# Kernel tuning notes

Measured on AMD Instinct MI355X. Metric: run time of the kernel, lower is better.

The kernel has to match this reference:

```python
import jax, jax.numpy as jnp
import numpy as np


def setup_inputs() -> dict:
    key = jax.random.key(0)
    ks = jax.random.split(key, 8)
    B, C, D, H, W = 4, 256, 16, 16, 16
    C8 = C // 8
    x = jax.random.normal(ks[0], (B, C, D, H, W), dtype=jnp.float32)
    # 1x1x1 conv weights == per-channel linear maps
    Wq = jax.random.normal(ks[1], (C8, C), dtype=jnp.float32) * (1.0 / np.sqrt(C))
    bq = jax.random.normal(ks[2], (C8,), dtype=jnp.float32) * 0.01
    Wk = jax.random.normal(ks[3], (C8, C), dtype=jnp.float32) * (1.0 / np.sqrt(C))
    bk = jax.random.normal(ks[4], (C8,), dtype=jnp.float32) * 0.01
    Wv = jax.random.normal(ks[5], (C, C), dtype=jnp.float32) * (1.0 / np.sqrt(C))
    bv = jax.random.normal(ks[6], (C,), dtype=jnp.float32) * 0.01
    gamma = jax.random.normal(ks[7], (1,), dtype=jnp.float32) * 0.1
    return {"x": x, "Wq": Wq, "bq": bq, "Wk": Wk, "bk": bk,
            "Wv": Wv, "bv": bv, "gamma": gamma}


def reference(x, Wq, bq, Wk, bk, Wv, bv, gamma):
    B, C, D, H, W = x.shape
    N = D * H * W
    xf = x.reshape(B, C, N)  # (B, C, N)
    # 1x1x1 convs == channel-wise linear projections
    q = jnp.einsum('qc,bcn->bnq', Wq, xf) + bq            # (B, N, C/8)
    k = jnp.einsum('kc,bcn->bkn', Wk, xf) + bk[:, None]   # (B, C/8, N)
    v = jnp.einsum('vc,bcn->bvn', Wv, xf) + bv[:, None]   # (B, C, N)
    energy = jnp.einsum('bnc,bcm->bnm', q, k)             # (B, N, N), NO 1/sqrt(d) scaling (as in source)
    attention = jax.nn.softmax(energy, axis=-1)           # softmax over keys
    # out[b,c,m] = sum_n V[b,c,n] * A[b,m,n]  (torch: bmm(V, A^T))
    out = jnp.einsum('bcn,bmn->bcm', v, attention)        # (B, C, N)
    out = out.reshape(B, C, D, H, W)
    return gamma[0] * out + x
```

## Files before the change

kernel.cpp:

```cpp
#include <hip/hip_runtime.h>
#include <hip/hip_bf16.h>
#include <math.h>

#define BATCH 4
#define CH    256
#define NPOS  4096
#define DQK   32
#define SHIFT 20.0f

typedef __attribute__((ext_vector_type(8))) short bf16x8;
typedef __attribute__((ext_vector_type(4))) float f32x4;

static __device__ __forceinline__ unsigned int pack_bf2(float a, float b) {
    __hip_bfloat162 h = __float22bfloat162_rn(make_float2(a, b));
    return *reinterpret_cast<unsigned int*>(&h);
}
static __device__ __forceinline__ unsigned short f2bf1(float f) {
    unsigned int u = __float_as_uint(f);
    u += 0x7fff + ((u >> 16) & 1);
    return (unsigned short)(u >> 16);
}
static __device__ __forceinline__ bf16x8 pack8(const float* v) {
    bf16x8 r;
    #pragma unroll
    for (int j = 0; j < 8; ++j) r[j] = (short)f2bf1(v[j]);
    return r;
}

static __device__ __forceinline__ void lds_barrier() {
    asm volatile("s_waitcnt lgkmcnt(0)" ::: "memory");
    __builtin_amdgcn_s_barrier();
    asm volatile("" ::: "memory");
}

__global__ __launch_bounds__(256) void qkv_proj_mfma(
    const float* __restrict__ x,
    const float* __restrict__ Wq, const float* __restrict__ bq,
    const float* __restrict__ Wk, const float* __restrict__ bk,
    const float* __restrict__ Wv, const float* __restrict__ bv,
    __hip_bfloat16* __restrict__ qb, __hip_bfloat16* __restrict__ kb,
    __hip_bfloat16* __restrict__ vb)
{
    const int tid  = threadIdx.x;
    const int wave = tid >> 6, lane = tid & 63;
    const int g    = lane >> 4, lm = lane & 15;
    const int n0   = blockIdx.x * 32;
    const int b    = blockIdx.y;
    const float* xb = x + (size_t)b * CH * NPOS;

    bf16x8 xf[2][8];
    #pragma unroll
    for (int nt = 0; nt < 2; ++nt)
        #pragma unroll
        for (int kt = 0; kt < 8; ++kt) {
            const float* p = xb + (32 * kt + 8 * g) * NPOS + n0 + 16 * nt + lm;
            float v[8];
            #pragma unroll
            for (int j = 0; j < 8; ++j) v[j] = p[j * NPOS];
            xf[nt][kt] = pack8(v);
        }

    #pragma unroll
    for (int s = 0; s < 5; ++s) {
        const int cot = wave * 5 + s;
        const float* Wsrc; const float* bsrc; int cbase; int kind;
        if (cot < 2)      { Wsrc = Wq; bsrc = bq; cbase = cot * 16;      kind = 0; }
        else if (cot < 4) { Wsrc = Wk; bsrc = bk; cbase = cot * 16 - 32; kind = 1; }
        else              { Wsrc = Wv; bsrc = bv; cbase = cot * 16 - 64; kind = 2; }

        bf16x8 wf[8];
        const float* wrow = Wsrc + (size_t)(cbase + lm) * CH;
        #pragma unroll
        for (int kt = 0; kt < 8; ++kt) {
            float4 wa = *(const float4*)(wrow + 32 * kt + 8 * g);
            float4 wc = *(const float4*)(wrow + 32 * kt + 8 * g + 4);
            float wv[8] = {wa.x, wa.y, wa.z, wa.w, wc.x, wc.y, wc.z, wc.w};
            wf[kt] = pack8(wv);
        }
        const float4 b4 = *(const float4*)(bsrc + cbase + 4 * g);
        f32x4 a0 = {b4.x, b4.y, b4.z, b4.w};
        f32x4 a1 = a0;
        #pragma unroll
        for (int kt = 0; kt < 8; ++kt) {
            a0 = __builtin_amdgcn_mfma_f32_16x16x32_bf16(wf[kt], xf[0][kt], a0, 0, 0, 0);
            a1 = __builtin_amdgcn_mfma_f32_16x16x32_bf16(wf[kt], xf[1][kt], a1, 0, 0, 0);
        }

        if (kind <= 1) {
            __hip_bfloat16* dst = (kind == 0 ? qb : kb);
            #pragma unroll
            for (int nt = 0; nt < 2; ++nt) {
                f32x4 a = nt ? a1 : a0;
                int n = n0 + 16 * nt + lm;
                uint2 w;
                w.x = pack_bf2(a[0], a[1]);
                w.y = pack_bf2(a[2], a[3]);
                *(uint2*)(dst + ((size_t)b * NPOS + n) * DQK + cbase + 4 * g) = w;
            }
        } else {
            #pragma unroll
            for (int nt = 0; nt < 2; ++nt) {
                f32x4 a = nt ? a1 : a0;
                int n = n0 + 16 * nt + lm;
                int n64 = n >> 6, half = (n >> 5) & 1, nin = n & 31;
                #pragma unroll
                for (int r = 0; r < 4; ++r) {
                    int c = cbase + 4 * g + r;
                    size_t off = (((size_t)b * 16 + (c >> 4)) * 64 + n64) * 1024
                               + (size_t)half * 512 + (c & 15) * 32 + nin;
                    *reinterpret_cast<unsigned short*>(vb + off) = f2bf1(a[r]);
                }
            }
        }
    }
}

__global__ __launch_bounds__(512) void flash_pam_kernel(
    const __hip_bfloat16* __restrict__ qb, const __hip_bfloat16* __restrict__ kb,
    const __hip_bfloat16* __restrict__ vb, const float* __restrict__ x,
    const float* __restrict__ gamma, float* __restrict__ out)
{
    __shared__ alignas(16) unsigned char Pl[2][8192];
    __shared__ float lred[4][4][16];

    const int tid  = threadIdx.x;
    const int wave = tid >> 6;
    const int lane = tid & 63;
    const int g    = lane >> 4;
    const int lm   = lane & 15;
    const int bid  = blockIdx.x;
    const int b    = bid & 3;
    const int m0   = (bid >> 2) * 64;
    const int kt   = wave & 3;
    const int mtA  = (wave >> 2) * 2;
    const unsigned swz = (unsigned)(lm & 7) << 4;

    const bf16x8 qfA = *reinterpret_cast<const bf16x8*>(
        qb + ((size_t)b * NPOS + m0 + 16 * mtA + lm) * DQK + 8 * g);
    const bf16x8 qfB = *reinterpret_cast<const bf16x8*>(
        qb + ((size_t)b * NPOS + m0 + 16 * mtA + 16 + lm) * DQK + 8 * g);

    const __hip_bfloat16* kbb = kb + (size_t)b * NPOS * DQK;
    const int koff0 = (16 * kt + lm) * DQK + 8 * g;
    const __hip_bfloat16* vbb = vb + (size_t)b * 16 * 64 * 1024;
    int vfb[4];
    #pragma unroll
    for (int cti = 0; cti < 2; ++cti)
        #pragma unroll
        for (int kc = 0; kc < 2; ++kc)
            vfb[2 * cti + kc] = (2 * wave + cti) * 65536 + kc * 512 + lm * 32 + 8 * g;

    const unsigned wbA = (unsigned)(16 * mtA + lm) * 128
                       + (((unsigned)(32 * kt + 8 * g)) ^ swz);
    const unsigned wbB = wbA + 16 * 128;

    unsigned char* P0 = &Pl[0][0];
    unsigned char* P1 = &Pl[1][0];

    f32x4 acc[2][4];
    #pragma unroll
    for (int i = 0; i < 2; ++i)
        #pragma unroll
        for (int j = 0; j < 4; ++j) acc[i][j] = (f32x4){0.f, 0.f, 0.f, 0.f};
    float lsA = 0.f, lsB = 0.f;

#define LOADK(dst, tk_) \
    dst = *reinterpret_cast<const bf16x8*>(kbb + koff0 + (tk_) * 2048);

#define LOADV(dst, tv_) { \
    _Pragma("unroll") for (int f = 0; f < 4; ++f) \
        dst[f] = *reinterpret_cast<const bf16x8*>(vbb + vfb[f] + (tv_) * 1024); }

#define QKW(KU, PW) { \
    f32x4 z = {0.f, 0.f, 0.f, 0.f}; \
    f32x4 sA = __builtin_amdgcn_mfma_f32_16x16x32_bf16(KU, qfA, z, 0, 0, 0); \
    f32x4 sB = __builtin_amdgcn_mfma_f32_16x16x32_bf16(KU, qfB, z, 0, 0, 0); \
    { float p0 = __expf(sA[0] - SHIFT), p1 = __expf(sA[1] - SHIFT); \
      float p2 = __expf(sA[2] - SHIFT), p3 = __expf(sA[3] - SHIFT); \
      lsA += (p0 + p1) + (p2 + p3); \
      uint2 w; w.x = pack_bf2(p0, p1); w.y = pack_bf2(p2, p3); \
      *reinterpret_cast<uint2*>((PW) + wbA) = w; } \
    { float p0 = __expf(sB[0] - SHIFT), p1 = __expf(sB[1] - SHIFT); \
      float p2 = __expf(sB[2] - SHIFT), p3 = __expf(sB[3] - SHIFT); \
      lsB += (p0 + p1) + (p2 + p3); \
      uint2 w; w.x = pack_bf2(p0, p1); w.y = pack_bf2(p2, p3); \
      *reinterpret_cast<uint2*>((PW) + wbB) = w; } }

#define PV(PR, VR) { \
    _Pragma("unroll") for (int kc = 0; kc < 2; ++kc) { \
        bf16x8 pf[4]; \
        _Pragma("unroll") for (int mt = 0; mt < 4; ++mt) \
            pf[mt] = *reinterpret_cast<const bf16x8*>( \
                (PR) + (unsigned)(16 * mt + lm) * 128 \
                     + (((unsigned)(kc * 64 + 16 * g)) ^ swz)); \
        __builtin_amdgcn_s_setprio(1); \
        _Pragma("unroll") for (int cti = 0; cti < 2; ++cti) \
            _Pragma("unroll") for (int mt = 0; mt < 4; ++mt) \
                acc[cti][mt] = __builtin_amdgcn_mfma_f32_16x16x32_bf16( \
                    VR[2 * cti + kc], pf[mt], acc[cti][mt], 0, 0, 0); \
        __builtin_amdgcn_s_setprio(0); } }

#define BODY(t_, PR, PW, VR, VL, KU, KL) { \
    { int tv = (t_) + 1; if (tv > 63) tv = 63; LOADV(VL, tv); } \
    { int tk2 = (t_) + 2; if (tk2 > 63) tk2 = 63; LOADK(KL, tk2); } \
    QKW(KU, PW); \
    PV(PR, VR); \
    lds_barrier(); }

    bf16x8 kA, kB, vA[4], vB[4];
    LOADK(kA, 0);
    LOADV(vA, 0);
    LOADK(kB, 1);
    QKW(kA, P0);
    lds_barrier();

    for (int it = 0; it < 31; ++it) {
        BODY(2 * it,     P0, P1, vA, vB, kB, kA);
        BODY(2 * it + 1, P1, P0, vB, vA, kA, kB);
    }
    BODY(62, P0, P1, vA, vB, kB, kA);
    PV(P1, vB);

    lsA += __shfl_xor(lsA, 16); lsA += __shfl_xor(lsA, 32);
    lsB += __shfl_xor(lsB, 16); lsB += __shfl_xor(lsB, 32);
    if (lane < 16) {
        lred[kt][mtA][lm]     = lsA;
        lred[kt][mtA + 1][lm] = lsB;
    }
    __syncthreads();

    float linv[4];
    #pragma unroll
    for (int mt = 0; mt < 4; ++mt)
        linv[mt] = 1.f / (lred[0][mt][lm] + lred[1][mt][lm]
                        + lred[2][mt][lm] + lred[3][mt][lm]);

    const float gmv = gamma[0];
    #pragma unroll
    for (int cti = 0; cti < 2; ++cti)
        #pragma unroll
        for (int mt = 0; mt < 4; ++mt)
            #pragma unroll
            for (int r = 0; r < 4; ++r) {
                int c = 32 * wave + 16 * cti + 4 * g + r;
                size_t idx = ((size_t)b * CH + c) * NPOS + m0 + 16 * mt + lm;
                out[idx] = gmv * (acc[cti][mt][r] * linv[mt]) + x[idx];
            }
#undef BODY
#undef PV
#undef QKW
#undef LOADV
#undef LOADK
}

extern "C" void kernel_launch(void* const* d_in, const int* in_sizes, int n_in,
                              void* d_out, int out_size, void* d_ws, size_t ws_size,
                              hipStream_t stream) {
    const float* x  = (const float*)d_in[0];
    const float* Wq = (const float*)d_in[1];
    const float* bq = (const float*)d_in[2];
    const float* Wk = (const float*)d_in[3];
    const float* bk = (const float*)d_in[4];
    const float* Wv = (const float*)d_in[5];
    const float* bv = (const float*)d_in[6];
    const float* gm = (const float*)d_in[7];
    float* out = (float*)d_out;

    __hip_bfloat16* qbuf = (__hip_bfloat16*)d_ws;
    __hip_bfloat16* kbuf = qbuf + (size_t)BATCH * NPOS * DQK;
    __hip_bfloat16* vbuf = kbuf + (size_t)BATCH * NPOS * DQK;

    qkv_proj_mfma<<<dim3(NPOS / 32, BATCH), 256, 0, stream>>>(
        x, Wq, bq, Wk, bk, Wv, bv, qbuf, kbuf, vbuf);
    flash_pam_kernel<<<dim3(NPOS / 64 * BATCH), 512, 0, stream>>>(
        qbuf, kbuf, vbuf, x, gm, out);
}
```

Baseline: 75.10 us.

## Process two key tiles per barrier with doubled P buffers

The flash-attention main loop now handles two 64-key tiles per iteration. It writes both P tiles into a doubled LDS buffer and runs both PV passes before a single barrier, which halves the number of barriers per key. K is prefetched further ahead, and V tiles for the next pair are loaded in advance. This uses more LDS and more registers for the extra V/K prefetch buffers, which may lower occupancy or cause spills.

After: 77.14 us. 2.7% more time.

```diff
diff --git a/kernel.cpp b/kernel.cpp
--- a/kernel.cpp
+++ b/kernel.cpp
@@ -120,7 +120,7 @@
     const __hip_bfloat16* __restrict__ vb, const float* __restrict__ x,
     const float* __restrict__ gamma, float* __restrict__ out)
 {
-    __shared__ alignas(16) unsigned char Pl[2][8192];
+    __shared__ alignas(16) unsigned char Pl[2][2][8192];
     __shared__ float lred[4][4][16];
 
     const int tid  = threadIdx.x;
@@ -154,8 +154,8 @@
                        + (((unsigned)(32 * kt + 8 * g)) ^ swz);
     const unsigned wbB = wbA + 16 * 128;
 
-    unsigned char* P0 = &Pl[0][0];
-    unsigned char* P1 = &Pl[1][0];
+    unsigned char* P0 = &Pl[0][0][0];
+    unsigned char* P1 = &Pl[1][0][0];
 
     f32x4 acc[2][4];
     #pragma unroll
@@ -167,7 +167,7 @@
 #define LOADK(dst, tk_) \
     dst = *reinterpret_cast<const bf16x8*>(kbb + koff0 + (tk_) * 2048);
 
-#define LOADV(dst, tv_) { \
+#define LOADV4(dst, tv_) { \
     _Pragma("unroll") for (int f = 0; f < 4; ++f) \
         dst[f] = *reinterpret_cast<const bf16x8*>(vbb + vfb[f] + (tv_) * 1024); }
 
@@ -186,13 +186,13 @@
       uint2 w; w.x = pack_bf2(p0, p1); w.y = pack_bf2(p2, p3); \
       *reinterpret_cast<uint2*>((PW) + wbB) = w; } }
 
-#define PV(PR, VR) { \
+#define PVt(PRb, VR) { \
+    bf16x8 pf[4]; \
     _Pragma("unroll") for (int kc = 0; kc < 2; ++kc) { \
-        bf16x8 pf[4]; \
         _Pragma("unroll") for (int mt = 0; mt < 4; ++mt) \
             pf[mt] = *reinterpret_cast<const bf16x8*>( \
-                (PR) + (unsigned)(16 * mt + lm) * 128 \
-                     + (((unsigned)(kc * 64 + 16 * g)) ^ swz)); \
+                (PRb) + (unsigned)(16 * mt + lm) * 128 \
+                      + (((unsigned)(kc * 64 + 16 * g)) ^ swz)); \
         __builtin_amdgcn_s_setprio(1); \
         _Pragma("unroll") for (int cti = 0; cti < 2; ++cti) \
             _Pragma("unroll") for (int mt = 0; mt < 4; ++mt) \
@@ -200,26 +200,33 @@
                     VR[2 * cti + kc], pf[mt], acc[cti][mt], 0, 0, 0); \
         __builtin_amdgcn_s_setprio(0); } }
 
-#define BODY(t_, PR, PW, VR, VL, KU, KL) { \
-    { int tv = (t_) + 1; if (tv > 63) tv = 63; LOADV(VL, tv); } \
-    { int tk2 = (t_) + 2; if (tk2 > 63) tk2 = 63; LOADK(KL, tk2); } \
-    QKW(KU, PW); \
-    PV(PR, VR); \
+#define BODY2(t_, PR, PW, VRa, VRb, VLa, VLb, KU0, KU1, KL0, KL1) { \
+    LOADV4(VLa, (t_) + 2); \
+    LOADV4(VLb, (t_) + 3); \
+    { int tk = (t_) + 4; if (tk > 63) tk = 63; LOADK(KL0, tk); } \
+    { int tk = (t_) + 5; if (tk > 63) tk = 63; LOADK(KL1, tk); } \
+    QKW(KU0, PW); \
+    QKW(KU1, (PW) + 8192); \
+    PVt(PR, VRa); \
+    PVt((PR) + 8192, VRb); \
     lds_barrier(); }
 
-    bf16x8 kA, kB, vA[4], vB[4];
-    LOADK(kA, 0);
-    LOADV(vA, 0);
-    LOADK(kB, 1);
-    QKW(kA, P0);
+    bf16x8 k0, k1, k2, k3, vA0[4], vA1[4], vB0[4], vB1[4];
+    LOADK(k0, 0); LOADK(k1, 1);
+    LOADV4(vA0, 0); LOADV4(vA1, 1);
+    LOADK(k2, 2); LOADK(k3, 3);
+    QKW(k0, P0);
+    QKW(k1, P0 + 8192);
     lds_barrier();
 
-    for (int it = 0; it < 31; ++it) {
-        BODY(2 * it,     P0, P1, vA, vB, kB, kA);
-        BODY(2 * it + 1, P1, P0, vB, vA, kA, kB);
+    for (int it = 0; it < 15; ++it) {
+        const int t4 = 4 * it;
+        BODY2(t4,     P0, P1, vA0, vA1, vB0, vB1, k2, k3, k0, k1);
+        BODY2(t4 + 2, P1, P0, vB0, vB1, vA0, vA1, k0, k1, k2, k3);
     }
-    BODY(62, P0, P1, vA, vB, kB, kA);
-    PV(P1, vB);
+    BODY2(60, P0, P1, vA0, vA1, vB0, vB1, k2, k3, k0, k1);
+    PVt(P1, vB0);
+    PVt(P1 + 8192, vB1);
 
     lsA += __shfl_xor(lsA, 16); lsA += __shfl_xor(lsA, 32);
     lsB += __shfl_xor(lsB, 16); lsB += __shfl_xor(lsB, 32);
@@ -246,10 +253,10 @@
                 size_t idx = ((size_t)b * CH + c) * NPOS + m0 + 16 * mt + lm;
                 out[idx] = gmv * (acc[cti][mt][r] * linv[mt]) + x[idx];
             }
-#undef BODY
-#undef PV
+#undef BODY2
+#undef PVt
 #undef QKW
-#undef LOADV
+#undef LOADV4
 #undef LOADK
 }
 
```

## Stage K/V tiles via global_load_lds DMA and fold softmax shift into exp2

Applied to the files above, without the earlier changes.

Replaces the register-prefetched K and V loads in the flash kernel with direct global-to-LDS DMA (global_load_lds) into per-wave staging buffers, which are then read back from LDS each iteration. The aim is to cut VGPR pressure from the double-buffered register prefetch and let the DMA overlap compute. Separately, Q is pre-scaled by log2(e) in the projection kernel and the softmax shift is folded into the MFMA accumulator init, so exp becomes a bare exp2 with no subtraction. The costs are extra LDS use (about 40KB), a vmcnt(0) wait at the top of each iteration that exposes load latency, and a single-buffered staging area.

Measured after the change: 82.24 us. 1.1x slower.

```diff
diff --git a/kernel.cpp b/kernel.cpp
--- a/kernel.cpp
+++ b/kernel.cpp
@@ -6,7 +6,8 @@
 #define CH    256
 #define NPOS  4096
 #define DQK   32
-#define SHIFT 20.0f
+#define LOG2E 1.4426950408889634f
+#define QB2   (-28.853900817779268f)
 
 typedef __attribute__((ext_vector_type(8))) short bf16x8;
 typedef __attribute__((ext_vector_type(4))) float f32x4;
@@ -31,6 +32,16 @@
     asm volatile("s_waitcnt lgkmcnt(0)" ::: "memory");
     __builtin_amdgcn_s_barrier();
     asm volatile("" ::: "memory");
+}
+#define VWAIT0() do { asm volatile("s_waitcnt vmcnt(0)" ::: "memory"); \
+                      __builtin_amdgcn_sched_barrier(0); } while (0)
+#define LGKM0()  do { asm volatile("s_waitcnt lgkmcnt(0)" ::: "memory"); \
+                      __builtin_amdgcn_sched_barrier(0); } while (0)
+
+static __device__ __forceinline__ void dma16(const __hip_bfloat16* g, unsigned char* l) {
+    __builtin_amdgcn_global_load_lds(
+        (const __attribute__((address_space(1))) void*)g,
+        (__attribute__((address_space(3))) void*)l, 16, 0, 0);
 }
 
 __global__ __launch_bounds__(256) void qkv_proj_mfma(
@@ -85,6 +96,10 @@
             a0 = __builtin_amdgcn_mfma_f32_16x16x32_bf16(wf[kt], xf[0][kt], a0, 0, 0, 0);
             a1 = __builtin_amdgcn_mfma_f32_16x16x32_bf16(wf[kt], xf[1][kt], a1, 0, 0, 0);
         }
+        if (kind == 0) {
+            #pragma unroll
+            for (int r = 0; r < 4; ++r) { a0[r] *= LOG2E; a1[r] *= LOG2E; }
+        }
 
         if (kind <= 1) {
             __hip_bfloat16* dst = (kind == 0 ? qb : kb);
@@ -121,6 +136,8 @@
     const float* __restrict__ gamma, float* __restrict__ out)
 {
     __shared__ alignas(16) unsigned char Pl[2][8192];
+    __shared__ alignas(16) unsigned char Vst[8][4096];
+    __shared__ alignas(16) unsigned char Kst[8][1024];
     __shared__ float lred[4][4][16];
 
     const int tid  = threadIdx.x;
@@ -134,26 +151,27 @@
     const int kt   = wave & 3;
     const int mtA  = (wave >> 2) * 2;
     const unsigned swz = (unsigned)(lm & 7) << 4;
+    const unsigned lane16 = (unsigned)lane * 16;
 
     const bf16x8 qfA = *reinterpret_cast<const bf16x8*>(
         qb + ((size_t)b * NPOS + m0 + 16 * mtA + lm) * DQK + 8 * g);
     const bf16x8 qfB = *reinterpret_cast<const bf16x8*>(
         qb + ((size_t)b * NPOS + m0 + 16 * mtA + 16 + lm) * DQK + 8 * g);
 
-    const __hip_bfloat16* kbb = kb + (size_t)b * NPOS * DQK;
-    const int koff0 = (16 * kt + lm) * DQK + 8 * g;
+    const __hip_bfloat16* kgl = kb + (size_t)b * NPOS * DQK + (16 * kt + lm) * DQK + 8 * g;
     const __hip_bfloat16* vbb = vb + (size_t)b * 16 * 64 * 1024;
-    int vfb[4];
+    const __hip_bfloat16* vgl[4];
     #pragma unroll
     for (int cti = 0; cti < 2; ++cti)
         #pragma unroll
         for (int kc = 0; kc < 2; ++kc)
-            vfb[2 * cti + kc] = (2 * wave + cti) * 65536 + kc * 512 + lm * 32 + 8 * g;
+            vgl[2 * cti + kc] = vbb + (2 * wave + cti) * 65536 + kc * 512 + lm * 32 + 8 * g;
+    unsigned char* vdst = &Vst[wave][0];
+    unsigned char* kdst = &Kst[wave][0];
 
     const unsigned wbA = (unsigned)(16 * mtA + lm) * 128
                        + (((unsigned)(32 * kt + 8 * g)) ^ swz);
     const unsigned wbB = wbA + 16 * 128;
-
     unsigned char* P0 = &Pl[0][0];
     unsigned char* P1 = &Pl[1][0];
 
@@ -164,29 +182,31 @@
         for (int j = 0; j < 4; ++j) acc[i][j] = (f32x4){0.f, 0.f, 0.f, 0.f};
     float lsA = 0.f, lsB = 0.f;
 
-#define LOADK(dst, tk_) \
-    dst = *reinterpret_cast<const bf16x8*>(kbb + koff0 + (tk_) * 2048);
-
-#define LOADV(dst, tv_) { \
+#define DMAK(t_) dma16(kgl + (size_t)(t_) * 2048, kdst)
+#define DMAV(t_) { \
     _Pragma("unroll") for (int f = 0; f < 4; ++f) \
-        dst[f] = *reinterpret_cast<const bf16x8*>(vbb + vfb[f] + (tv_) * 1024); }
+        dma16(vgl[f] + (size_t)(t_) * 1024, vdst + f * 1024); }
+#define READK(dst) dst = *reinterpret_cast<const bf16x8*>(kdst + lane16);
+#define READV(dst) { \
+    _Pragma("unroll") for (int f = 0; f < 4; ++f) \
+        dst[f] = *reinterpret_cast<const bf16x8*>(vdst + f * 1024 + lane16); }
 
 #define QKW(KU, PW) { \
-    f32x4 z = {0.f, 0.f, 0.f, 0.f}; \
-    f32x4 sA = __builtin_amdgcn_mfma_f32_16x16x32_bf16(KU, qfA, z, 0, 0, 0); \
-    f32x4 sB = __builtin_amdgcn_mfma_f32_16x16x32_bf16(KU, qfB, z, 0, 0, 0); \
-    { float p0 = __expf(sA[0] - SHIFT), p1 = __expf(sA[1] - SHIFT); \
-      float p2 = __expf(sA[2] - SHIFT), p3 = __expf(sA[3] - SHIFT); \
+    f32x4 zb = {QB2, QB2, QB2, QB2}; \
+    f32x4 sA = __builtin_amdgcn_mfma_f32_16x16x32_bf16(KU, qfA, zb, 0, 0, 0); \
+    f32x4 sB = __builtin_amdgcn_mfma_f32_16x16x32_bf16(KU, qfB, zb, 0, 0, 0); \
+    { float p0 = exp2f(sA[0]), p1 = exp2f(sA[1]); \
+      float p2 = exp2f(sA[2]), p3 = exp2f(sA[3]); \
       lsA += (p0 + p1) + (p2 + p3); \
       uint2 w; w.x = pack_bf2(p0, p1); w.y = pack_bf2(p2, p3); \
       *reinterpret_cast<uint2*>((PW) + wbA) = w; } \
-    { float p0 = __expf(sB[0] - SHIFT), p1 = __expf(sB[1] - SHIFT); \
-      float p2 = __expf(sB[2] - SHIFT), p3 = __expf(sB[3] - SHIFT); \
+    { float p0 = exp2f(sB[0]), p1 = exp2f(sB[1]); \
+      float p2 = exp2f(sB[2]), p3 = exp2f(sB[3]); \
       lsB += (p0 + p1) + (p2 + p3); \
       uint2 w; w.x = pack_bf2(p0, p1); w.y = pack_bf2(p2, p3); \
       *reinterpret_cast<uint2*>((PW) + wbB) = w; } }
 
-#define PV(PR, VR) { \
+#define PVt(PR, VR) { \
     _Pragma("unroll") for (int kc = 0; kc < 2; ++kc) { \
         bf16x8 pf[4]; \
         _Pragma("unroll") for (int mt = 0; mt < 4; ++mt) \
@@ -200,26 +220,37 @@
                     VR[2 * cti + kc], pf[mt], acc[cti][mt], 0, 0, 0); \
         __builtin_amdgcn_s_setprio(0); } }
 
-#define BODY(t_, PR, PW, VR, VL, KU, KL) { \
-    { int tv = (t_) + 1; if (tv > 63) tv = 63; LOADV(VL, tv); } \
-    { int tk2 = (t_) + 2; if (tk2 > 63) tk2 = 63; LOADK(KL, tk2); } \
-    QKW(KU, PW); \
-    PV(PR, VR); \
+#define BODY(t_, PR, PW) { \
+    VWAIT0(); \
+    bf16x8 kreg; READK(kreg); \
+    bf16x8 vreg[4]; READV(vreg); \
+    LGKM0(); \
+    DMAV((t_) + 1); \
+    { int tk2 = (t_) + 2; if (tk2 > 63) tk2 = 63; DMAK(tk2); } \
+    QKW(kreg, PW); \
+    PVt(PR, vreg); \
     lds_barrier(); }
 
-    bf16x8 kA, kB, vA[4], vB[4];
-    LOADK(kA, 0);
-    LOADV(vA, 0);
-    LOADK(kB, 1);
-    QKW(kA, P0);
+    DMAK(0);
+    VWAIT0();
+    bf16x8 k0; READK(k0);
+    LGKM0();
+    DMAV(0);
+    DMAK(1);
+    QKW(k0, P0);
     lds_barrier();
 
     for (int it = 0; it < 31; ++it) {
-        BODY(2 * it,     P0, P1, vA, vB, kB, kA);
-        BODY(2 * it + 1, P1, P0, vB, vA, kA, kB);
+        BODY(2 * it,     P0, P1);
+        BODY(2 * it + 1, P1, P0);
     }
-    BODY(62, P0, P1, vA, vB, kB, kA);
-    PV(P1, vB);
+    BODY(62, P0, P1);
+
+    VWAIT0();
+    {
+        bf16x8 vreg[4]; READV(vreg);
+        PVt(P1, vreg);
+    }
 
     lsA += __shfl_xor(lsA, 16); lsA += __shfl_xor(lsA, 32);
     lsB += __shfl_xor(lsB, 16); lsB += __shfl_xor(lsB, 32);
@@ -247,10 +278,12 @@
                 out[idx] = gmv * (acc[cti][mt][r] * linv[mt]) + x[idx];
             }
 #undef BODY
-#undef PV
+#undef PVt
 #undef QKW
-#undef LOADV
-#undef LOADK
+#undef READV
+#undef READK
+#undef DMAV
+#undef DMAK
 }
 
 extern "C" void kernel_launch(void* const* d_in, const int* in_sizes, int n_in,
```

## Pre-convert weights to bf16, stage x via LDS, fold log2e into Q, hoist P loads

Applied to the files above, without the earlier changes.

Adds a small kernel that converts the Q/K/V projection weights to bf16 once per call, with log2(e) folded into Q's weights and bias, so the projection no longer converts them repeatedly. The projection kernel now loads x rows with coalesced float4 reads into a swizzled LDS tile instead of strided per-element global reads. In the attention loop the softmax shift is moved into the MFMA accumulator init and exp2f replaces __expf, and all P fragment LDS reads are hoisted to the start of each iteration ahead of the QK work. The cost is an extra kernel launch and higher register pressure from holding eight P fragments across the QK step.

After: 72.77 us. 1.03x faster.

```diff
diff --git a/kernel.cpp b/kernel.cpp
--- a/kernel.cpp
+++ b/kernel.cpp
@@ -6,7 +6,8 @@
 #define CH    256
 #define NPOS  4096
 #define DQK   32
-#define SHIFT 20.0f
+#define LOG2E 1.4426950408889634f
+#define QB2   (-28.853900817779268f)
 
 typedef __attribute__((ext_vector_type(8))) short bf16x8;
 typedef __attribute__((ext_vector_type(4))) float f32x4;
@@ -20,12 +21,6 @@
     u += 0x7fff + ((u >> 16) & 1);
     return (unsigned short)(u >> 16);
 }
-static __device__ __forceinline__ bf16x8 pack8(const float* v) {
-    bf16x8 r;
-    #pragma unroll
-    for (int j = 0; j < 8; ++j) r[j] = (short)f2bf1(v[j]);
-    return r;
-}
 
 static __device__ __forceinline__ void lds_barrier() {
     asm volatile("s_waitcnt lgkmcnt(0)" ::: "memory");
@@ -33,51 +28,82 @@
     asm volatile("" ::: "memory");
 }
 
-__global__ __launch_bounds__(256) void qkv_proj_mfma(
-    const float* __restrict__ x,
+__global__ __launch_bounds__(256) void conv_w(
     const float* __restrict__ Wq, const float* __restrict__ bq,
     const float* __restrict__ Wk, const float* __restrict__ bk,
     const float* __restrict__ Wv, const float* __restrict__ bv,
+    __hip_bfloat16* __restrict__ Wbf, float* __restrict__ bcat)
+{
+    const int co = blockIdx.x;
+    const int ci = threadIdx.x;
+    const float* src; float scale = 1.f;
+    if (co < 32)      { src = Wq + (size_t)co * 256;        scale = LOG2E; }
+    else if (co < 64) { src = Wk + (size_t)(co - 32) * 256; }
+    else              { src = Wv + (size_t)(co - 64) * 256; }
+    *reinterpret_cast<unsigned short*>(Wbf + (size_t)co * 256 + ci) =
+        f2bf1(src[ci] * scale);
+    if (ci == 0)
+        bcat[co] = co < 32 ? bq[co] * LOG2E
+                 : (co < 64 ? bk[co - 32] : bv[co - 64]);
+}
+
+__global__ __launch_bounds__(256) void qkv_proj_mfma(
+    const float* __restrict__ x,
+    const __hip_bfloat16* __restrict__ Wbf, const float* __restrict__ bcat,
     __hip_bfloat16* __restrict__ qb, __hip_bfloat16* __restrict__ kb,
     __hip_bfloat16* __restrict__ vb)
 {
+    __shared__ alignas(16) unsigned char Xl[16384];
     const int tid  = threadIdx.x;
     const int wave = tid >> 6, lane = tid & 63;
     const int g    = lane >> 4, lm = lane & 15;
     const int n0   = blockIdx.x * 32;
     const int b    = blockIdx.y;
-    const float* xb = x + (size_t)b * CH * NPOS;
+
+    {
+        const int c   = tid;
+        const int ktc = c >> 5, gc = (c >> 3) & 3, jc = c & 7;
+        const unsigned xw = (unsigned)(4 * ktc + gc);
+        const float* xp = x + ((size_t)b * CH + c) * NPOS + n0;
+        #pragma unroll
+        for (int i = 0; i < 8; ++i) {
+            const float4 v4 = reinterpret_cast<const float4*>(xp)[i];
+            const float vv[4] = {v4.x, v4.y, v4.z, v4.w};
+            #pragma unroll
+            for (int e = 0; e < 4; ++e) {
+                const int nrel = 4 * i + e;
+                const unsigned off =
+                    (unsigned)(((nrel >> 4) * 8 + ktc) * 1024)
+                  + ((((unsigned)(gc * 16 + (nrel & 15))) ^ xw) * 16)
+                  + (unsigned)(jc * 2);
+                *reinterpret_cast<unsigned short*>(Xl + off) = f2bf1(vv[e]);
+            }
+        }
+    }
+    __syncthreads();
 
     bf16x8 xf[2][8];
     #pragma unroll
     for (int nt = 0; nt < 2; ++nt)
         #pragma unroll
         for (int kt = 0; kt < 8; ++kt) {
-            const float* p = xb + (32 * kt + 8 * g) * NPOS + n0 + 16 * nt + lm;
-            float v[8];
-            #pragma unroll
-            for (int j = 0; j < 8; ++j) v[j] = p[j * NPOS];
-            xf[nt][kt] = pack8(v);
+            const unsigned slot = (unsigned)lane ^ (unsigned)(4 * kt + g);
+            xf[nt][kt] = *reinterpret_cast<const bf16x8*>(
+                Xl + (unsigned)((nt * 8 + kt) * 1024) + slot * 16);
         }
 
     #pragma unroll
     for (int s = 0; s < 5; ++s) {
         const int cot = wave * 5 + s;
-        const float* Wsrc; const float* bsrc; int cbase; int kind;
-        if (cot < 2)      { Wsrc = Wq; bsrc = bq; cbase = cot * 16;      kind = 0; }
-        else if (cot < 4) { Wsrc = Wk; bsrc = bk; cbase = cot * 16 - 32; kind = 1; }
-        else              { Wsrc = Wv; bsrc = bv; cbase = cot * 16 - 64; kind = 2; }
+        const int cog = cot * 16;
 
         bf16x8 wf[8];
-        const float* wrow = Wsrc + (size_t)(cbase + lm) * CH;
-        #pragma unroll
-        for (int kt = 0; kt < 8; ++kt) {
-            float4 wa = *(const float4*)(wrow + 32 * kt + 8 * g);
-            float4 wc = *(const float4*)(wrow + 32 * kt + 8 * g + 4);
-            float wv[8] = {wa.x, wa.y, wa.z, wa.w, wc.x, wc.y, wc.z, wc.w};
-            wf[kt] = pack8(wv);
-        }
-        const float4 b4 = *(const float4*)(bsrc + cbase + 4 * g);
+        const __hip_bfloat16* wrow = Wbf + (size_t)(cog + lm) * 256;
+        #pragma unroll
+        for (int kt = 0; kt < 8; ++kt)
+            wf[kt] = *reinterpret_cast<const bf16x8*>(wrow + 32 * kt + 8 * g);
+
+        const float4 b4 = *reinterpret_cast<const float4*>(bcat + cog + 4 * g);
         f32x4 a0 = {b4.x, b4.y, b4.z, b4.w};
         f32x4 a1 = a0;
         #pragma unroll
@@ -86,8 +112,9 @@
             a1 = __builtin_amdgcn_mfma_f32_16x16x32_bf16(wf[kt], xf[1][kt], a1, 0, 0, 0);
         }
 
-        if (kind <= 1) {
-            __hip_bfloat16* dst = (kind == 0 ? qb : kb);
+        if (cot < 4) {
+            __hip_bfloat16* dst = (cot < 2 ? qb : kb);
+            const int cb = (cot < 2 ? cot * 16 : cot * 16 - 32);
             #pragma unroll
             for (int nt = 0; nt < 2; ++nt) {
                 f32x4 a = nt ? a1 : a0;
@@ -95,9 +122,10 @@
                 uint2 w;
                 w.x = pack_bf2(a[0], a[1]);
                 w.y = pack_bf2(a[2], a[3]);
-                *(uint2*)(dst + ((size_t)b * NPOS + n) * DQK + cbase + 4 * g) = w;
+                *(uint2*)(dst + ((size_t)b * NPOS + n) * DQK + cb + 4 * g) = w;
             }
         } else {
+            const int cbase = cot * 16 - 64;
             #pragma unroll
             for (int nt = 0; nt < 2; ++nt) {
                 f32x4 a = nt ? a1 : a0;
@@ -172,21 +200,21 @@
         dst[f] = *reinterpret_cast<const bf16x8*>(vbb + vfb[f] + (tv_) * 1024); }
 
 #define QKW(KU, PW) { \
-    f32x4 z = {0.f, 0.f, 0.f, 0.f}; \
-    f32x4 sA = __builtin_amdgcn_mfma_f32_16x16x32_bf16(KU, qfA, z, 0, 0, 0); \
-    f32x4 sB = __builtin_amdgcn_mfma_f32_16x16x32_bf16(KU, qfB, z, 0, 0, 0); \
-    { float p0 = __expf(sA[0] - SHIFT), p1 = __expf(sA[1] - SHIFT); \
-      float p2 = __expf(sA[2] - SHIFT), p3 = __expf(sA[3] - SHIFT); \
+    f32x4 zb = {QB2, QB2, QB2, QB2}; \
+    f32x4 sA = __builtin_amdgcn_mfma_f32_16x16x32_bf16(KU, qfA, zb, 0, 0, 0); \
+    f32x4 sB = __builtin_amdgcn_mfma_f32_16x16x32_bf16(KU, qfB, zb, 0, 0, 0); \
+    { float p0 = exp2f(sA[0]), p1 = exp2f(sA[1]); \
+      float p2 = exp2f(sA[2]), p3 = exp2f(sA[3]); \
       lsA += (p0 + p1) + (p2 + p3); \
       uint2 w; w.x = pack_bf2(p0, p1); w.y = pack_bf2(p2, p3); \
       *reinterpret_cast<uint2*>((PW) + wbA) = w; } \
-    { float p0 = __expf(sB[0] - SHIFT), p1 = __expf(sB[1] - SHIFT); \
-      float p2 = __expf(sB[2] - SHIFT), p3 = __expf(sB[3] - SHIFT); \
+    { float p0 = exp2f(sB[0]), p1 = exp2f(sB[1]); \
+      float p2 = exp2f(sB[2]), p3 = exp2f(sB[3]); \
       lsB += (p0 + p1) + (p2 + p3); \
       uint2 w; w.x = pack_bf2(p0, p1); w.y = pack_bf2(p2, p3); \
       *reinterpret_cast<uint2*>((PW) + wbB) = w; } }
 
-#define PV(PR, VR) { \
+#define PVt(PR, VR) { \
     _Pragma("unroll") for (int kc = 0; kc < 2; ++kc) { \
         bf16x8 pf[4]; \
         _Pragma("unroll") for (int mt = 0; mt < 4; ++mt) \
@@ -201,10 +229,22 @@
         __builtin_amdgcn_s_setprio(0); } }
 
 #define BODY(t_, PR, PW, VR, VL, KU, KL) { \
+    bf16x8 pf[2][4]; \
+    _Pragma("unroll") for (int kc = 0; kc < 2; ++kc) \
+        _Pragma("unroll") for (int mt = 0; mt < 4; ++mt) \
+            pf[kc][mt] = *reinterpret_cast<const bf16x8*>( \
+                (PR) + (unsigned)(16 * mt + lm) * 128 \
+                     + (((unsigned)(kc * 64 + 16 * g)) ^ swz)); \
     { int tv = (t_) + 1; if (tv > 63) tv = 63; LOADV(VL, tv); } \
     { int tk2 = (t_) + 2; if (tk2 > 63) tk2 = 63; LOADK(KL, tk2); } \
     QKW(KU, PW); \
-    PV(PR, VR); \
+    __builtin_amdgcn_s_setprio(1); \
+    _Pragma("unroll") for (int kc = 0; kc < 2; ++kc) \
+        _Pragma("unroll") for (int cti = 0; cti < 2; ++cti) \
+            _Pragma("unroll") for (int mt = 0; mt < 4; ++mt) \
+                acc[cti][mt] = __builtin_amdgcn_mfma_f32_16x16x32_bf16( \
+                    VR[2 * cti + kc], pf[kc][mt], acc[cti][mt], 0, 0, 0); \
+    __builtin_amdgcn_s_setprio(0); \
     lds_barrier(); }
 
     bf16x8 kA, kB, vA[4], vB[4];
@@ -219,7 +259,7 @@
         BODY(2 * it + 1, P1, P0, vB, vA, kA, kB);
     }
     BODY(62, P0, P1, vA, vB, kB, kA);
-    PV(P1, vB);
+    PVt(P1, vB);
 
     lsA += __shfl_xor(lsA, 16); lsA += __shfl_xor(lsA, 32);
     lsB += __shfl_xor(lsB, 16); lsB += __shfl_xor(lsB, 32);
@@ -247,7 +287,7 @@
                 out[idx] = gmv * (acc[cti][mt][r] * linv[mt]) + x[idx];
             }
 #undef BODY
-#undef PV
+#undef PVt
 #undef QKW
 #undef LOADV
 #undef LOADK
@@ -269,9 +309,12 @@
     __hip_bfloat16* qbuf = (__hip_bfloat16*)d_ws;
     __hip_bfloat16* kbuf = qbuf + (size_t)BATCH * NPOS * DQK;
     __hip_bfloat16* vbuf = kbuf + (size_t)BATCH * NPOS * DQK;
-
+    __hip_bfloat16* wbf  = vbuf + (size_t)BATCH * CH * NPOS;
+    float* bcat = (float*)(wbf + 320 * 256);
+
+    conv_w<<<dim3(320), 256, 0, stream>>>(Wq, bq, Wk, bk, Wv, bv, wbf, bcat);
     qkv_proj_mfma<<<dim3(NPOS / 32, BATCH), 256, 0, stream>>>(
-        x, Wq, bq, Wk, bk, Wv, bv, qbuf, kbuf, vbuf);
+        x, wbf, bcat, qbuf, kbuf, vbuf);
     flash_pam_kernel<<<dim3(NPOS / 64 * BATCH), 512, 0, stream>>>(
         qbuf, kbuf, vbuf, x, gm, out);
 }
```
